# Kernel optimization log

Hardware: AMD Instinct MI355X
Metric: run time of the kernel (lower is better)

## Reference

```python
import jax, jax.numpy as jnp
import numpy as np

N_HEADS = 8

def setup_inputs() -> dict:
    key = jax.random.key(0)
    ks = jax.random.split(key, 5)
    C = 256
    x = jax.random.normal(ks[0], (4, C, 48, 48), dtype=jnp.float32)
    w_qkv = jax.random.normal(ks[1], (3 * C, C), dtype=jnp.float32) * (C ** -0.5)
    b_qkv = jax.random.normal(ks[2], (3 * C,), dtype=jnp.float32) * 0.02
    w_proj = jax.random.normal(ks[3], (C, C), dtype=jnp.float32) * (C ** -0.5)
    b_proj = jax.random.normal(ks[4], (C,), dtype=jnp.float32) * 0.02
    return {"x": x, "w_qkv": w_qkv, "b_qkv": b_qkv, "w_proj": w_proj, "b_proj": b_proj}


def reference(x, w_qkv, b_qkv, w_proj, b_proj):
    B, C, H, W = x.shape
    h = N_HEADS
    dh = C // h
    N = H * W
    # flatten spatial dims to tokens: [B, N, C]
    xf = x.reshape(B, C, N).transpose(0, 2, 1)
    # fused qkv projection (torch Linear: y = x @ W.T + b)
    qkv = xf @ w_qkv.T + b_qkv                      # [B, N, 3C]
    qkv = qkv.reshape(B, N, 3, h, dh).transpose(2, 0, 3, 1, 4)  # [3, B, h, N, dh]
    q, k, v = qkv[0], qkv[1], qkv[2]
    scale = dh ** -0.5
    attn = jax.nn.softmax(jnp.einsum('bhnd,bhmd->bhnm', q, k) * scale, axis=-1)
    out = jnp.einsum('bhnm,bhmd->bhnd', attn, v)    # [B, h, N, dh]
    out = out.transpose(0, 2, 1, 3).reshape(B, N, C)
    out = out @ w_proj.T + b_proj                   # [B, N, C]
    return out.transpose(0, 2, 1).reshape(B, C, H, W)
```

## Files before the change

### kernel.cpp

```cpp
#include <hip/hip_runtime.h>
#include <hip/hip_bf16.h>

#define B_    4
#define C_    256
#define NTOK  2304
#define NH    8
#define DH    32

typedef short bf16x8 __attribute__((ext_vector_type(8)));
typedef short bf16x4 __attribute__((ext_vector_type(4)));
typedef float f32x4  __attribute__((ext_vector_type(4)));

__device__ __forceinline__ short rne_bf16(float f) {
    union { float f; unsigned u; } v; v.f = f;
    const unsigned r = v.u + 0x7fffu + ((v.u >> 16) & 1u);
    return (short)(r >> 16);
}
__device__ __forceinline__ unsigned pack2_bf16(float a, float b) {
    return (unsigned)(unsigned short)rne_bf16(a) | ((unsigned)(unsigned short)rne_bf16(b) << 16);
}
__device__ __forceinline__ float fast_exp2(float x) {
#if __has_builtin(__builtin_amdgcn_exp2f)
    return __builtin_amdgcn_exp2f(x);
#else
    return exp2f(x);
#endif
}

__global__ __launch_bounds__(256) void prep_kernel(
    const float* __restrict__ x, const float* __restrict__ wq,
    const float* __restrict__ wp,
    short* __restrict__ xt, short* __restrict__ wqb, short* __restrict__ wpb)
{
    const int blk = blockIdx.x;
    const int t   = threadIdx.x;
    if (blk < 576) {
        const int b  = blk / 144;
        const int rem = blk % 144;
        const int n0 = (rem / 4) * 64;
        const int c0 = (rem % 4) * 64;
        __shared__ float tile[64][65];
        const float* xb = x + ((size_t)b * C_ + c0) * NTOK + n0;
        const int n = t & 63, cc = t >> 6;
        #pragma unroll
        for (int r = 0; r < 16; ++r)
            tile[cc + r * 4][n] = xb[(size_t)(cc + r * 4) * NTOK + n];
        __syncthreads();
        const int nr = t >> 2, cb = (t & 3) * 16;
        short* dst = xt + ((size_t)b * NTOK + n0 + nr) * C_ + c0 + cb;
        bf16x8 v0, v1;
        #pragma unroll
        for (int u = 0; u < 8; ++u) v0[u] = rne_bf16(tile[cb + u][nr]);
        #pragma unroll
        for (int u = 0; u < 8; ++u) v1[u] = rne_bf16(tile[cb + 8 + u][nr]);
        *(bf16x8*)dst = v0;
        *(bf16x8*)(dst + 8) = v1;
    } else {
        const int id = (blk - 576) * 256 + t;
        const int base = id * 16;
        #pragma unroll
        for (int u = 0; u < 4; ++u) {
            const int off = base + u * 4;
            float4 v; short* d;
            if (off < 196608) { v = *(const float4*)(wq + off); d = wqb + off; }
            else { v = *(const float4*)(wp + (off - 196608)); d = wpb + (off - 196608); }
            d[0] = rne_bf16(v.x); d[1] = rne_bf16(v.y);
            d[2] = rne_bf16(v.z); d[3] = rne_bf16(v.w);
        }
    }
}

__global__ __launch_bounds__(256) void qkv_mfma(
    const short* __restrict__ xt,
    const short* __restrict__ wqb,
    const float* __restrict__ bias,
    short* __restrict__ qb, short* __restrict__ kb, short* __restrict__ vt)
{
    __shared__ short Es[4][2560];
    const int wave = threadIdx.x >> 6;
    const int lane = threadIdx.x & 63;
    const int quad = lane >> 4, l16 = lane & 15;
    const int wid  = blockIdx.x * 4 + wave;
    const int b    = wid / 864;
    const int rem  = wid % 864;
    const int mt = rem / 12, nt = rem % 12;
    const int m0 = mt * 32, j0 = nt * 64;

    const short* abase = xt + ((size_t)b * NTOK + m0 + l16) * C_ + quad * 8;
    const short* bbase = wqb + (size_t)(j0 + l16) * C_ + quad * 8;

    f32x4 acc[2][4] = {};
    for (int k0 = 0; k0 < C_; k0 += 32) {
        bf16x8 af[2], bfr[4];
        #pragma unroll
        for (int i = 0; i < 2; ++i)
            af[i] = *(const bf16x8*)(abase + (size_t)i * 16 * C_ + k0);
        #pragma unroll
        for (int j = 0; j < 4; ++j)
            bfr[j] = *(const bf16x8*)(bbase + (size_t)j * 16 * C_ + k0);
        #pragma unroll
        for (int i = 0; i < 2; ++i)
            #pragma unroll
            for (int j = 0; j < 4; ++j)
                acc[i][j] = __builtin_amdgcn_mfma_f32_16x16x32_bf16(af[i], bfr[j], acc[i][j], 0, 0, 0);
    }

    short* Ew = Es[wave];
    const int three = j0 >> 8;
    if (three < 2) {
        const float sc = (three == 0) ? 0.25503486f : 1.0f;
        #pragma unroll
        for (int j = 0; j < 4; ++j) {
            const float bv = bias[j0 + j * 16 + l16];
            #pragma unroll
            for (int i = 0; i < 2; ++i)
                #pragma unroll
                for (int r = 0; r < 4; ++r) {
                    const int n_l = i * 16 + quad * 4 + r;
                    Ew[n_l * 72 + j * 16 + l16] = rne_bf16((acc[i][j][r] + bv) * sc);
                }
        }
        const int n_l = lane & 31, hh = lane >> 5;
        const int head = ((j0 + hh * 32) >> 5) & 7;
        short* dst = ((three == 0) ? qb : kb)
                   + ((size_t)(b * NH + head) * NTOK + m0 + n_l) * DH;
        #pragma unroll
        for (int s = 0; s < 4; ++s)
            *(bf16x8*)(dst + s * 8) = *(const bf16x8*)&Ew[n_l * 72 + hh * 32 + s * 8];
    } else {
        #pragma unroll
        for (int j = 0; j < 4; ++j) {
            const float bv = bias[j0 + j * 16 + l16];
            const int j_l = j * 16 + l16;
            #pragma unroll
            for (int i = 0; i < 2; ++i) {
                const int nb = i * 16 + quad * 4;
                *(unsigned*)&Ew[j_l * 40 + nb] =
                    pack2_bf16(acc[i][j][0] + bv, acc[i][j][1] + bv);
                *(unsigned*)&Ew[j_l * 40 + nb + 2] =
                    pack2_bf16(acc[i][j][2] + bv, acc[i][j][3] + bv);
            }
        }
        #pragma unroll
        for (int p = 0; p < 4; ++p) {
            const int j_r = p * 16 + (lane >> 2);
            const int seg = (lane & 3) * 8;
            const int head = ((j0 + j_r) >> 5) & 7;
            const int d    = j_r & 31;
            *(bf16x8*)(vt + ((size_t)(b * NH + head) * DH + d) * NTOK + m0 + seg) =
                *(const bf16x8*)&Ew[j_r * 40 + seg];
        }
    }
}

__global__ __launch_bounds__(256) void attn_kernel(
    const short* __restrict__ qg,
    const short* __restrict__ kg,
    const short* __restrict__ vg,
    float* __restrict__ po,
    float* __restrict__ pl)
{
    const int bh   = blockIdx.y;
    const int q0   = blockIdx.x * 64;
    const int half = blockIdx.z;
    const int t    = threadIdx.x;
    const int wave = t >> 6;
    const int lane = t & 63;
    const int quad = lane >> 4;
    const int l16  = lane & 15;

    __shared__ short Ks[64][40];
    __shared__ short Vt[32][72];
    __shared__ short Ps[4][16][68];

    const short* kbase = kg + (size_t)bh * NTOK * DH;
    const short* vbase = vg + (size_t)bh * DH * NTOK;

    const short* qptr = qg + ((size_t)bh * NTOK + q0 + wave * 16 + l16) * DH + quad * 8;
    const bf16x8 qf = *(const bf16x8*)qptr;

    f32x4 Oc0 = {0.f, 0.f, 0.f, 0.f};
    f32x4 Oc1 = {0.f, 0.f, 0.f, 0.f};
    float lpart[4] = {0.f, 0.f, 0.f, 0.f};

    const int kbeg = half * (NTOK / 2);
    const int kend = kbeg + (NTOK / 2);

    const int kr = t >> 2, ksg = t & 3;
    const int vr = t >> 3, vsg = t & 7;

    bf16x8 kreg = *(const bf16x8*)(kbase + (size_t)(kbeg + kr) * DH + ksg * 8);
    bf16x8 vreg = *(const bf16x8*)(vbase + (size_t)vr * NTOK + kbeg + vsg * 8);

    for (int kt = kbeg; kt < kend; kt += 64) {
        *(bf16x8*)&Ks[kr][ksg * 8] = kreg;
        *(bf16x8*)&Vt[vr][vsg * 8] = vreg;
        __syncthreads();

        const int ktn = (kt + 64 < kend) ? kt + 64 : kbeg;
        kreg = *(const bf16x8*)(kbase + (size_t)(ktn + kr) * DH + ksg * 8);
        vreg = *(const bf16x8*)(vbase + (size_t)vr * NTOK + ktn + vsg * 8);

        f32x4 S[4];
        #pragma unroll
        for (int jt = 0; jt < 4; ++jt) {
            const bf16x8 kf = *(const bf16x8*)&Ks[jt * 16 + l16][quad * 8];
            f32x4 z = {0.f, 0.f, 0.f, 0.f};
            S[jt] = __builtin_amdgcn_mfma_f32_16x16x32_bf16(qf, kf, z, 0, 0, 0);
        }

        #pragma unroll
        for (int jt = 0; jt < 4; ++jt) {
            #pragma unroll
            for (int r = 0; r < 4; ++r) {
                const float p = fast_exp2(S[jt][r]);
                lpart[r] += p;
                Ps[wave][quad * 4 + r][jt * 16 + l16] = rne_bf16(p);
            }
        }

        #pragma unroll
        for (int jc = 0; jc < 2; ++jc) {
            const bf16x4 p0 = *(const bf16x4*)&Ps[wave][l16][jc * 32 + quad * 8];
            const bf16x4 p1 = *(const bf16x4*)&Ps[wave][l16][jc * 32 + quad * 8 + 4];
            bf16x8 af;
            af[0] = p0[0]; af[1] = p0[1]; af[2] = p0[2]; af[3] = p0[3];
            af[4] = p1[0]; af[5] = p1[1]; af[6] = p1[2]; af[7] = p1[3];
            const bf16x8 b0 = *(const bf16x8*)&Vt[l16][jc * 32 + quad * 8];
            const bf16x8 b1 = *(const bf16x8*)&Vt[16 + l16][jc * 32 + quad * 8];
            Oc0 = __builtin_amdgcn_mfma_f32_16x16x32_bf16(af, b0, Oc0, 0, 0, 0);
            Oc1 = __builtin_amdgcn_mfma_f32_16x16x32_bf16(af, b1, Oc1, 0, 0, 0);
        }
        __syncthreads();
    }

    #pragma unroll
    for (int off = 1; off < 16; off <<= 1) {
        #pragma unroll
        for (int r = 0; r < 4; ++r)
            lpart[r] += __shfl_xor(lpart[r], off, 64);
    }

    const size_t rowbase = ((size_t)half * 32 + bh) * NTOK + q0 + wave * 16 + quad * 4;
    float* obase = po + rowbase * DH + l16;
    #pragma unroll
    for (int r = 0; r < 4; ++r) {
        obase[(size_t)r * DH]      = Oc0[r];
        obase[(size_t)r * DH + 16] = Oc1[r];
    }
    if (l16 == 0) {
        float* lb = pl + rowbase;
        #pragma unroll
        for (int r = 0; r < 4; ++r) lb[r] = lpart[r];
    }
}

__global__ __launch_bounds__(256) void proj_mfma(
    const float* __restrict__ po,
    const float* __restrict__ pl,
    const short* __restrict__ wpb,
    const float* __restrict__ bias,
    float* __restrict__ out)
{
    __shared__ float Ep[4][2304];
    const int wave = threadIdx.x >> 6;
    const int lane = threadIdx.x & 63;
    const int quad = lane >> 4, l16 = lane & 15;
    const int wid  = blockIdx.x * 4 + wave;
    const int b    = wid / 288;
    const int rem  = wid % 288;
    const int mt = rem / 4, ct = rem % 4;
    const int m0 = mt * 32, c0 = ct * 64;

    const short* bbase = wpb + (size_t)(c0 + l16) * C_ + quad * 8;
    const size_t PO_OFF = (size_t)32 * NTOK * DH;
    const size_t PL_OFF = (size_t)32 * NTOK;

    f32x4 acc[2][4] = {};
    for (int kt = 0; kt < 8; ++kt) {
        bf16x8 af[2], bfr[4];
        #pragma unroll
        for (int i = 0; i < 2; ++i) {
            const size_t row = (size_t)(b * NH + kt) * NTOK + m0 + i * 16 + l16;
            const float inv = 1.f / (pl[row] + pl[PL_OFF + row]);
            const float* p0 = po + row * DH + quad * 8;
            const f32x4 a0 = *(const f32x4*)p0;
            const f32x4 a1 = *(const f32x4*)(p0 + 4);
            const f32x4 b0 = *(const f32x4*)(p0 + PO_OFF);
            const f32x4 b1 = *(const f32x4*)(p0 + PO_OFF + 4);
            #pragma unroll
            for (int u = 0; u < 4; ++u) {
                af[i][u]     = rne_bf16((a0[u] + b0[u]) * inv);
                af[i][4 + u] = rne_bf16((a1[u] + b1[u]) * inv);
            }
        }
        #pragma unroll
        for (int j = 0; j < 4; ++j)
            bfr[j] = *(const bf16x8*)(bbase + (size_t)j * 16 * C_ + kt * 32);
        #pragma unroll
        for (int i = 0; i < 2; ++i)
            #pragma unroll
            for (int j = 0; j < 4; ++j)
                acc[i][j] = __builtin_amdgcn_mfma_f32_16x16x32_bf16(af[i], bfr[j], acc[i][j], 0, 0, 0);
    }

    float* Ew = Ep[wave];
    #pragma unroll
    for (int j = 0; j < 4; ++j) {
        const int j_l = j * 16 + l16;
        const float bv = bias[c0 + j_l];
        #pragma unroll
        for (int i = 0; i < 2; ++i) {
            f32x4 st = {acc[i][j][0] + bv, acc[i][j][1] + bv,
                        acc[i][j][2] + bv, acc[i][j][3] + bv};
            *(f32x4*)&Ew[j_l * 36 + i * 16 + quad * 4] = st;
        }
    }
    #pragma unroll
    for (int p = 0; p < 8; ++p) {
        const int c_r = p * 8 + (lane >> 3);
        const int seg = (lane & 7) * 4;
        *(float4*)(out + ((size_t)b * C_ + c0 + c_r) * NTOK + m0 + seg) =
            *(const float4*)&Ew[c_r * 36 + seg];
    }
}

extern "C" void kernel_launch(void* const* d_in, const int* in_sizes, int n_in,
                              void* d_out, int out_size, void* d_ws, size_t ws_size,
                              hipStream_t stream) {
    const float* x      = (const float*)d_in[0];
    const float* w_qkv  = (const float*)d_in[1];
    const float* b_qkv  = (const float*)d_in[2];
    const float* w_proj = (const float*)d_in[3];
    const float* b_proj = (const float*)d_in[4];
    float* out = (float*)d_out;

    const size_t SZ = (size_t)B_ * NH * NTOK * DH;
    short* xt  = (short*)d_ws;
    short* wqb = xt + SZ;
    short* wpb = wqb + 196608;
    short* qb  = wpb + 65536;
    short* kb  = qb + SZ;
    short* vt  = kb + SZ;
    float* po  = (float*)(vt + SZ);
    float* pl  = po + 2 * SZ;

    prep_kernel<<<640, 256, 0, stream>>>(x, w_qkv, w_proj, xt, wqb, wpb);
    qkv_mfma<<<864, 256, 0, stream>>>(xt, wqb, b_qkv, qb, kb, vt);
    attn_kernel<<<dim3(36, 32, 2), 256, 0, stream>>>(qb, kb, vt, po, pl);
    proj_mfma<<<288, 256, 0, stream>>>(po, pl, wpb, b_proj, out);
}
```

Before: 173.6 us.

## Fuse x transpose/cast into QKV GEMM and stage normalized attention output in LDS

The separate transpose-and-cast pass over x is removed. The QKV GEMM block now loads its 32-token fp32 slice of x directly, converts it to bf16 and stores it transposed in shared memory, where four waves covering different output column tiles share it. The projection kernel similarly stages the combined, normalized attention partials for all heads once per block into LDS instead of each wave recomputing them. This cuts one kernel's global round trip and redundant loads, at the cost of extra LDS use and a block barrier per GEMM block.

New measurement: 159.5 us. 1.09x faster.

```diff
diff --git a/kernel.cpp b/kernel.cpp
--- a/kernel.cpp
+++ b/kernel.cpp
@@ -28,65 +28,59 @@
 }
 
 __global__ __launch_bounds__(256) void prep_kernel(
-    const float* __restrict__ x, const float* __restrict__ wq,
-    const float* __restrict__ wp,
-    short* __restrict__ xt, short* __restrict__ wqb, short* __restrict__ wpb)
+    const float* __restrict__ wq, const float* __restrict__ wp,
+    short* __restrict__ wqb, short* __restrict__ wpb)
 {
-    const int blk = blockIdx.x;
-    const int t   = threadIdx.x;
-    if (blk < 576) {
-        const int b  = blk / 144;
-        const int rem = blk % 144;
-        const int n0 = (rem / 4) * 64;
-        const int c0 = (rem % 4) * 64;
-        __shared__ float tile[64][65];
-        const float* xb = x + ((size_t)b * C_ + c0) * NTOK + n0;
-        const int n = t & 63, cc = t >> 6;
-        #pragma unroll
-        for (int r = 0; r < 16; ++r)
-            tile[cc + r * 4][n] = xb[(size_t)(cc + r * 4) * NTOK + n];
-        __syncthreads();
-        const int nr = t >> 2, cb = (t & 3) * 16;
-        short* dst = xt + ((size_t)b * NTOK + n0 + nr) * C_ + c0 + cb;
-        bf16x8 v0, v1;
-        #pragma unroll
-        for (int u = 0; u < 8; ++u) v0[u] = rne_bf16(tile[cb + u][nr]);
-        #pragma unroll
-        for (int u = 0; u < 8; ++u) v1[u] = rne_bf16(tile[cb + 8 + u][nr]);
-        *(bf16x8*)dst = v0;
-        *(bf16x8*)(dst + 8) = v1;
-    } else {
-        const int id = (blk - 576) * 256 + t;
-        const int base = id * 16;
-        #pragma unroll
-        for (int u = 0; u < 4; ++u) {
-            const int off = base + u * 4;
-            float4 v; short* d;
-            if (off < 196608) { v = *(const float4*)(wq + off); d = wqb + off; }
-            else { v = *(const float4*)(wp + (off - 196608)); d = wpb + (off - 196608); }
-            d[0] = rne_bf16(v.x); d[1] = rne_bf16(v.y);
-            d[2] = rne_bf16(v.z); d[3] = rne_bf16(v.w);
-        }
+    const int id = blockIdx.x * 256 + threadIdx.x;
+    const int base = id * 16;
+    #pragma unroll
+    for (int u = 0; u < 4; ++u) {
+        const int off = base + u * 4;
+        float4 v; short* d;
+        if (off < 196608) { v = *(const float4*)(wq + off); d = wqb + off; }
+        else { v = *(const float4*)(wp + (off - 196608)); d = wpb + (off - 196608); }
+        d[0] = rne_bf16(v.x); d[1] = rne_bf16(v.y);
+        d[2] = rne_bf16(v.z); d[3] = rne_bf16(v.w);
     }
 }
 
 __global__ __launch_bounds__(256) void qkv_mfma(
-    const short* __restrict__ xt,
+    const float* __restrict__ x,
     const short* __restrict__ wqb,
     const float* __restrict__ bias,
     short* __restrict__ qb, short* __restrict__ kb, short* __restrict__ vt)
 {
+    __shared__ short As[32][264];
     __shared__ short Es[4][2560];
-    const int wave = threadIdx.x >> 6;
-    const int lane = threadIdx.x & 63;
+    const int t    = threadIdx.x;
+    const int wave = t >> 6;
+    const int lane = t & 63;
     const int quad = lane >> 4, l16 = lane & 15;
-    const int wid  = blockIdx.x * 4 + wave;
-    const int b    = wid / 864;
-    const int rem  = wid % 864;
-    const int mt = rem / 12, nt = rem % 12;
-    const int m0 = mt * 32, j0 = nt * 64;
-
-    const short* abase = xt + ((size_t)b * NTOK + m0 + l16) * C_ + quad * 8;
+    const int blk  = blockIdx.x;
+    const int b    = blk / 216;
+    const int rem  = blk % 216;
+    const int mt   = rem / 3;
+    const int jg   = rem % 3;
+    const int m0   = mt * 32;
+    const int j0   = (jg * 4 + wave) * 64;
+
+    {
+        const int n4  = (t & 7) * 4;
+        const int tc2 = t >> 3;
+        const float* xb = x + ((size_t)b * C_) * NTOK + m0 + n4;
+        #pragma unroll
+        for (int r = 0; r < 4; ++r) {
+            const int c = tc2 * 2 + r * 64;
+            const float4 v0 = *(const float4*)(xb + (size_t)c * NTOK);
+            const float4 v1 = *(const float4*)(xb + (size_t)(c + 1) * NTOK);
+            *(unsigned*)&As[n4 + 0][c] = pack2_bf16(v0.x, v1.x);
+            *(unsigned*)&As[n4 + 1][c] = pack2_bf16(v0.y, v1.y);
+            *(unsigned*)&As[n4 + 2][c] = pack2_bf16(v0.z, v1.z);
+            *(unsigned*)&As[n4 + 3][c] = pack2_bf16(v0.w, v1.w);
+        }
+    }
+    __syncthreads();
+
     const short* bbase = wqb + (size_t)(j0 + l16) * C_ + quad * 8;
 
     f32x4 acc[2][4] = {};
@@ -94,7 +88,7 @@
         bf16x8 af[2], bfr[4];
         #pragma unroll
         for (int i = 0; i < 2; ++i)
-            af[i] = *(const bf16x8*)(abase + (size_t)i * 16 * C_ + k0);
+            af[i] = *(const bf16x8*)&As[i * 16 + l16][k0 + quad * 8];
         #pragma unroll
         for (int j = 0; j < 4; ++j)
             bfr[j] = *(const bf16x8*)(bbase + (size_t)j * 16 * C_ + k0);
@@ -262,38 +256,46 @@
     const float* __restrict__ bias,
     float* __restrict__ out)
 {
+    __shared__ short Ac[32 * 336];
     __shared__ float Ep[4][2304];
-    const int wave = threadIdx.x >> 6;
-    const int lane = threadIdx.x & 63;
+    const int t    = threadIdx.x;
+    const int wave = t >> 6;
+    const int lane = t & 63;
     const int quad = lane >> 4, l16 = lane & 15;
-    const int wid  = blockIdx.x * 4 + wave;
-    const int b    = wid / 288;
-    const int rem  = wid % 288;
-    const int mt = rem / 4, ct = rem % 4;
-    const int m0 = mt * 32, c0 = ct * 64;
-
-    const short* bbase = wpb + (size_t)(c0 + l16) * C_ + quad * 8;
+    const int blk  = blockIdx.x;
+    const int b    = blk / 72;
+    const int mt   = blk % 72;
+    const int m0   = mt * 32;
+    const int c0   = wave * 64;
+
     const size_t PO_OFF = (size_t)32 * NTOK * DH;
     const size_t PL_OFF = (size_t)32 * NTOK;
+
+    {
+        const int m  = t >> 3;
+        const int d4 = (t & 7) * 4;
+        #pragma unroll
+        for (int h = 0; h < NH; ++h) {
+            const size_t row  = (size_t)(b * NH + h) * NTOK + m0 + m;
+            const float inv = 1.f / (pl[row] + pl[PL_OFF + row]);
+            const float* p0 = po + row * DH + d4;
+            const f32x4 a = *(const f32x4*)p0;
+            const f32x4 c = *(const f32x4*)(p0 + PO_OFF);
+            short* dst = &Ac[m * 336 + h * 40 + d4];
+            *(unsigned*)dst       = pack2_bf16((a[0] + c[0]) * inv, (a[1] + c[1]) * inv);
+            *(unsigned*)(dst + 2) = pack2_bf16((a[2] + c[2]) * inv, (a[3] + c[3]) * inv);
+        }
+    }
+    __syncthreads();
+
+    const short* bbase = wpb + (size_t)(c0 + l16) * C_ + quad * 8;
 
     f32x4 acc[2][4] = {};
     for (int kt = 0; kt < 8; ++kt) {
         bf16x8 af[2], bfr[4];
         #pragma unroll
-        for (int i = 0; i < 2; ++i) {
-            const size_t row = (size_t)(b * NH + kt) * NTOK + m0 + i * 16 + l16;
-            const float inv = 1.f / (pl[row] + pl[PL_OFF + row]);
-            const float* p0 = po + row * DH + quad * 8;
-            const f32x4 a0 = *(const f32x4*)p0;
-            const f32x4 a1 = *(const f32x4*)(p0 + 4);
-            const f32x4 b0 = *(const f32x4*)(p0 + PO_OFF);
-            const f32x4 b1 = *(const f32x4*)(p0 + PO_OFF + 4);
-            #pragma unroll
-            for (int u = 0; u < 4; ++u) {
-                af[i][u]     = rne_bf16((a0[u] + b0[u]) * inv);
-                af[i][4 + u] = rne_bf16((a1[u] + b1[u]) * inv);
-            }
-        }
+        for (int i = 0; i < 2; ++i)
+            af[i] = *(const bf16x8*)&Ac[(i * 16 + l16) * 336 + kt * 40 + quad * 8];
         #pragma unroll
         for (int j = 0; j < 4; ++j)
             bfr[j] = *(const bf16x8*)(bbase + (size_t)j * 16 * C_ + kt * 32);
@@ -336,8 +338,7 @@
     float* out = (float*)d_out;
 
     const size_t SZ = (size_t)B_ * NH * NTOK * DH;
-    short* xt  = (short*)d_ws;
-    short* wqb = xt + SZ;
+    short* wqb = (short*)d_ws;
     short* wpb = wqb + 196608;
     short* qb  = wpb + 65536;
     short* kb  = qb + SZ;
@@ -345,8 +346,8 @@
     float* po  = (float*)(vt + SZ);
     float* pl  = po + 2 * SZ;
 
-    prep_kernel<<<640, 256, 0, stream>>>(x, w_qkv, w_proj, xt, wqb, wpb);
-    qkv_mfma<<<864, 256, 0, stream>>>(xt, wqb, b_qkv, qb, kb, vt);
+    prep_kernel<<<64, 256, 0, stream>>>(w_qkv, w_proj, wqb, wpb);
+    qkv_mfma<<<864, 256, 0, stream>>>(x, wqb, b_qkv, qb, kb, vt);
     attn_kernel<<<dim3(36, 32, 2), 256, 0, stream>>>(qb, kb, vt, po, pl);
     proj_mfma<<<288, 256, 0, stream>>>(po, pl, wpb, b_proj, out);
 }
```
